# Optimization experiments

Hardware: AMD Instinct MI355X
Metric: run time of the kernel (lower is better)

The kernel has to match this reference:

```python
import jax, jax.numpy as jnp
import numpy as np

NQ, NK, D, DV = 8192, 2048, 2048, 2048

def setup_inputs() -> dict:
    key = jax.random.key(0)
    kq, kk, kv, km = jax.random.split(key, 4)
    Query = jax.random.normal(kq, (NQ, D), dtype=jnp.float32)
    Key = jax.random.normal(kk, (NK, D), dtype=jnp.float32)
    Value = jax.random.normal(kv, (NK, DV), dtype=jnp.float32)
    # binary multiplicative mask (keep prob 0.5); row-all-zero has negligible probability at NK=2048
    mask = (jax.random.uniform(km, (NQ, NK)) > 0.5).astype(jnp.float32)
    return {"Query": Query, "Key": Key, "Value": Value, "mask": mask}

def reference(Query, Key, Value, mask):
    d = Key.shape[1]
    scale = 1.0 / jnp.sqrt(jnp.asarray(d, dtype=Query.dtype))
    scores = jnp.einsum('qd,kd->qk', Query, Key) * scale  # [Nq, Nk]
    energy = jax.nn.softmax(scores, axis=-1) * mask
    att = energy / jnp.sum(energy, axis=-1, keepdims=True)  # renormalize after mask
    return jnp.einsum('qk,kv->qv', att, Value)
```

## Files before the change

### kernel.cpp

```cpp
#include <hip/hip_runtime.h>
#include <hip/hip_bf16.h>


#define NQ 8192
#define NK 2048
#define DD 2048
#define DVV 2048

typedef __attribute__((ext_vector_type(8))) short short8;
typedef __attribute__((ext_vector_type(4))) float f32x4;

typedef __attribute__((address_space(3))) void as3_void;
typedef __attribute__((address_space(1))) const void as1_cvoid;
#define GLOAD16(g, l) __builtin_amdgcn_global_load_lds((as1_cvoid*)(g), (as3_void*)(l), 16, 0, 0)

__global__ __launch_bounds__(256) void conv_bf16_kernel(
    __hip_bfloat16* __restrict__ dst, const float* __restrict__ src, int n4)
{
    int stride = gridDim.x * blockDim.x;
    for (int i = blockIdx.x * blockDim.x + threadIdx.x; i < n4; i += stride) {
        float4 f = reinterpret_cast<const float4*>(src)[i];
        union { __hip_bfloat16 h[4]; uint2 u; } p;
        p.h[0] = __float2bfloat16(f.x);
        p.h[1] = __float2bfloat16(f.y);
        p.h[2] = __float2bfloat16(f.z);
        p.h[3] = __float2bfloat16(f.w);
        reinterpret_cast<uint2*>(dst)[i] = p.u;
    }
}

__global__ __launch_bounds__(256) void transpose_conv_kernel(
    __hip_bfloat16* __restrict__ Vt, const float* __restrict__ V)
{
    __shared__ __hip_bfloat16 tile[64][65];
    const int tx = threadIdx.x;
    const int ty = threadIdx.y;
    const int r0 = blockIdx.y * 64;
    const int c0 = blockIdx.x * 64;
    #pragma unroll
    for (int j = ty; j < 64; j += 4)
        tile[j][tx] = __float2bfloat16(V[(size_t)(r0 + j) * DVV + c0 + tx]);
    __syncthreads();
    #pragma unroll
    for (int j = ty; j < 64; j += 4)
        Vt[(size_t)(c0 + j) * NK + r0 + tx] = tile[tx][j];
}

__global__ __launch_bounds__(256) void gemm_nt_kernel(
    float* __restrict__ C,
    const __hip_bfloat16* __restrict__ A,
    const __hip_bfloat16* __restrict__ B,
    int K, int lda, int ldb, int ldc, float scale)
{
    constexpr int BM = 128, BN = 128, BK = 64;
    __shared__ __align__(16) __hip_bfloat16 As[BM * BK];
    __shared__ __align__(16) __hip_bfloat16 Bs[BN * BK];

    const int tid  = threadIdx.x;
    const int wave = tid >> 6;
    const int lane = tid & 63;
    const int wm   = wave >> 1;
    const int wn   = wave & 1;
    const int bn   = blockIdx.x;
    const int bm   = blockIdx.y;

    f32x4 acc[4][4];
    #pragma unroll
    for (int i = 0; i < 4; ++i)
        #pragma unroll
        for (int j = 0; j < 4; ++j)
            acc[i][j] = (f32x4){0.f, 0.f, 0.f, 0.f};

    const int arow = tid >> 3;
    const int acol = (tid & 7) * 8;
    const __hip_bfloat16* Abase = A + (size_t)(bm * BM + arow) * lda + acol;
    const __hip_bfloat16* Bbase = B + (size_t)(bn * BN + arow) * ldb + acol;

    const int fr = lane & 15;
    const int kb = (lane >> 4) << 3;

    for (int kt = 0; kt < K; kt += BK) {
        __syncthreads();
        #pragma unroll
        for (int r = 0; r < 4; ++r) {
            GLOAD16(Abase + (size_t)(r * 32) * lda + kt, &As[(r * 256 + (wave << 6)) * 8]);
            GLOAD16(Bbase + (size_t)(r * 32) * ldb + kt, &Bs[(r * 256 + (wave << 6)) * 8]);
        }
        __syncthreads();

        #pragma unroll
        for (int kk = 0; kk < 2; ++kk) {
            short8 af[4], bfv[4];
            #pragma unroll
            for (int mi = 0; mi < 4; ++mi)
                af[mi] = *(const short8*)&As[(wm * 64 + mi * 16 + fr) * BK + kk * 32 + kb];
            #pragma unroll
            for (int ni = 0; ni < 4; ++ni)
                bfv[ni] = *(const short8*)&Bs[(wn * 64 + ni * 16 + fr) * BK + kk * 32 + kb];
            #pragma unroll
            for (int mi = 0; mi < 4; ++mi)
                #pragma unroll
                for (int ni = 0; ni < 4; ++ni)
                    acc[mi][ni] = __builtin_amdgcn_mfma_f32_16x16x32_bf16(
                        af[mi], bfv[ni], acc[mi][ni], 0, 0, 0);
        }
    }

    const int crow = bm * BM + wm * 64 + ((lane >> 4) << 2);
    const int ccol = bn * BN + wn * 64 + fr;
    #pragma unroll
    for (int mi = 0; mi < 4; ++mi)
        #pragma unroll
        for (int ni = 0; ni < 4; ++ni)
            #pragma unroll
            for (int r = 0; r < 4; ++r)
                C[(size_t)(crow + mi * 16 + r) * ldc + ccol + ni * 16] = acc[mi][ni][r] * scale;
}

__global__ __launch_bounds__(256) void softmax_mask_kernel(
    float* __restrict__ S, const float* __restrict__ mask)
{
    const int q    = blockIdx.x;
    const int t    = threadIdx.x;
    const int wave = t >> 6;
    const int lane = t & 63;

    const float4* srow = (const float4*)(S + (size_t)q * NK);
    const float4* mrow = (const float4*)(mask + (size_t)q * NK);
    float4 s0 = srow[t], s1 = srow[t + 256];
    float4 m0 = mrow[t], m1 = mrow[t + 256];

    float mx = fmaxf(fmaxf(fmaxf(s0.x, s0.y), fmaxf(s0.z, s0.w)),
                     fmaxf(fmaxf(s1.x, s1.y), fmaxf(s1.z, s1.w)));
    #pragma unroll
    for (int off = 32; off > 0; off >>= 1)
        mx = fmaxf(mx, __shfl_xor(mx, off));

    __shared__ float redm[4], reds[4];
    if (lane == 0) redm[wave] = mx;
    __syncthreads();
    mx = fmaxf(fmaxf(redm[0], redm[1]), fmaxf(redm[2], redm[3]));

    float e[8];
    e[0] = __expf(s0.x - mx) * m0.x;
    e[1] = __expf(s0.y - mx) * m0.y;
    e[2] = __expf(s0.z - mx) * m0.z;
    e[3] = __expf(s0.w - mx) * m0.w;
    e[4] = __expf(s1.x - mx) * m1.x;
    e[5] = __expf(s1.y - mx) * m1.y;
    e[6] = __expf(s1.z - mx) * m1.z;
    e[7] = __expf(s1.w - mx) * m1.w;

    float sum = ((e[0] + e[1]) + (e[2] + e[3])) + ((e[4] + e[5]) + (e[6] + e[7]));
    #pragma unroll
    for (int off = 32; off > 0; off >>= 1)
        sum += __shfl_xor(sum, off);
    if (lane == 0) reds[wave] = sum;
    __syncthreads();
    sum = (reds[0] + reds[1]) + (reds[2] + reds[3]);
    const float inv = 1.0f / sum;

    __hip_bfloat16* prow = reinterpret_cast<__hip_bfloat16*>(S) + (size_t)q * (2 * NK);
    union { __hip_bfloat16 h[4]; uint2 u; } p;
    p.h[0] = __float2bfloat16(e[0] * inv);
    p.h[1] = __float2bfloat16(e[1] * inv);
    p.h[2] = __float2bfloat16(e[2] * inv);
    p.h[3] = __float2bfloat16(e[3] * inv);
    reinterpret_cast<uint2*>(prow)[t] = p.u;
    p.h[0] = __float2bfloat16(e[4] * inv);
    p.h[1] = __float2bfloat16(e[5] * inv);
    p.h[2] = __float2bfloat16(e[6] * inv);
    p.h[3] = __float2bfloat16(e[7] * inv);
    reinterpret_cast<uint2*>(prow)[t + 256] = p.u;
}

extern "C" void kernel_launch(void* const* d_in, const int* in_sizes, int n_in,
                              void* d_out, int out_size, void* d_ws, size_t ws_size,
                              hipStream_t stream)
{
    const float* Q    = (const float*)d_in[0];
    const float* Km   = (const float*)d_in[1];
    const float* V    = (const float*)d_in[2];
    const float* mask = (const float*)d_in[3];
    float* out = (float*)d_out;

    char* ws = (char*)d_ws;
    __hip_bfloat16* Qb  = (__hip_bfloat16*)ws;
    __hip_bfloat16* Kb  = (__hip_bfloat16*)(ws + (size_t)32 * 1024 * 1024);
    __hip_bfloat16* Vtb = (__hip_bfloat16*)(ws + (size_t)40 * 1024 * 1024);
    float*          S   = (float*)        (ws + (size_t)48 * 1024 * 1024);

    conv_bf16_kernel<<<2048, 256, 0, stream>>>(Qb, Q, NQ * DD / 4);
    conv_bf16_kernel<<<1024, 256, 0, stream>>>(Kb, Km, NK * DD / 4);
    transpose_conv_kernel<<<dim3(DVV / 64, NK / 64), dim3(64, 4), 0, stream>>>(Vtb, V);

    const float scale = 0.022097086912079608f;
    gemm_nt_kernel<<<dim3(NK / 128, NQ / 128), 256, 0, stream>>>(
        S, Qb, Kb, DD, DD, DD, NK, scale);
    softmax_mask_kernel<<<NQ, 256, 0, stream>>>(S, mask);
    gemm_nt_kernel<<<dim3(DVV / 128, NQ / 128), 256, 0, stream>>>(
        out, (const __hip_bfloat16*)S, Vtb, NK, 2 * NK, NK, DVV, 1.0f);
}
```

Before: 394.4 us.

## Rewrite GEMM as 256x256 double-buffered 8-wave kernel with swizzled LDS

Replaces the 128x128 single-buffered GEMM with a 256x256 tile, 512-thread kernel that double-buffers LDS and interleaves global-to-LDS loads with MFMA quadrants, using XOR-swizzled LDS layout to avoid bank conflicts and a block-index swizzle for L2 locality. Aims to hide memory latency and raise arithmetic intensity per tile. Larger LDS footprint and register use reduce occupancy and add complexity in wait counts and barrier placement; the grid shrinks to 256 blocks, exactly one wave of work on the device.

After: 330.8 us. -16.1%, faster.

```diff
diff --git a/kernel.cpp b/kernel.cpp
--- a/kernel.cpp
+++ b/kernel.cpp
@@ -13,6 +13,9 @@
 typedef __attribute__((address_space(3))) void as3_void;
 typedef __attribute__((address_space(1))) const void as1_cvoid;
 #define GLOAD16(g, l) __builtin_amdgcn_global_load_lds((as1_cvoid*)(g), (as3_void*)(l), 16, 0, 0)
+
+#define SBAR do { __builtin_amdgcn_sched_barrier(0); __builtin_amdgcn_s_barrier(); } while (0)
+#define WLG0 do { asm volatile("s_waitcnt lgkmcnt(0)" ::: "memory"); __builtin_amdgcn_sched_barrier(0); } while (0)
 
 __global__ __launch_bounds__(256) void conv_bf16_kernel(
     __hip_bfloat16* __restrict__ dst, const float* __restrict__ src, int n4)
@@ -46,75 +49,143 @@
         Vt[(size_t)(c0 + j) * NK + r0 + tx] = tile[tx][j];
 }
 
-__global__ __launch_bounds__(256) void gemm_nt_kernel(
+__global__ __launch_bounds__(512, 2) void gemm_nt8_kernel(
     float* __restrict__ C,
     const __hip_bfloat16* __restrict__ A,
     const __hip_bfloat16* __restrict__ B,
     int K, int lda, int ldb, int ldc, float scale)
 {
-    constexpr int BM = 128, BN = 128, BK = 64;
-    __shared__ __align__(16) __hip_bfloat16 As[BM * BK];
-    __shared__ __align__(16) __hip_bfloat16 Bs[BN * BK];
+    constexpr int BM = 256, BN = 256, BK = 64;
+    const int NT = K / BK;
+    __shared__ __align__(16) __hip_bfloat16 As[2][BM * BK];
+    __shared__ __align__(16) __hip_bfloat16 Bs[2][BN * BK];
 
     const int tid  = threadIdx.x;
     const int wave = tid >> 6;
     const int lane = tid & 63;
-    const int wm   = wave >> 1;
-    const int wn   = wave & 1;
-    const int bn   = blockIdx.x;
-    const int bm   = blockIdx.y;
-
-    f32x4 acc[4][4];
-    #pragma unroll
-    for (int i = 0; i < 4; ++i)
+    const int wm   = wave >> 2;
+    const int wn   = wave & 3;
+    const int fr   = lane & 15;
+    const int fq   = lane >> 4;
+
+    const int swz = (blockIdx.x & 7) * 32 + (blockIdx.x >> 3);
+    const int bm  = swz >> 3;
+    const int bn  = swz & 7;
+
+    const int srow = tid >> 3;
+    const int scol = (((tid & 7) ^ (srow & 7)) << 3);
+
+    const __hip_bfloat16* Ab = A + (size_t)(bm * BM) * lda;
+    const __hip_bfloat16* Bb = B + (size_t)(bn * BN) * ldb;
+
+    f32x4 acc[8][4];
+    #pragma unroll
+    for (int i = 0; i < 8; ++i)
         #pragma unroll
         for (int j = 0; j < 4; ++j)
             acc[i][j] = (f32x4){0.f, 0.f, 0.f, 0.f};
 
-    const int arow = tid >> 3;
-    const int acol = (tid & 7) * 8;
-    const __hip_bfloat16* Abase = A + (size_t)(bm * BM + arow) * lda + acol;
-    const __hip_bfloat16* Bbase = B + (size_t)(bn * BN + arow) * ldb + acol;
-
-    const int fr = lane & 15;
-    const int kb = (lane >> 4) << 3;
-
-    for (int kt = 0; kt < K; kt += BK) {
-        __syncthreads();
-        #pragma unroll
-        for (int r = 0; r < 4; ++r) {
-            GLOAD16(Abase + (size_t)(r * 32) * lda + kt, &As[(r * 256 + (wave << 6)) * 8]);
-            GLOAD16(Bbase + (size_t)(r * 32) * ldb + kt, &Bs[(r * 256 + (wave << 6)) * 8]);
-        }
-        __syncthreads();
-
-        #pragma unroll
-        for (int kk = 0; kk < 2; ++kk) {
-            short8 af[4], bfv[4];
+    short8 af[4][2], b0[2][2], b1[2][2];
+
+    auto stage_a = [&](int pp, int h, int kt) {
+        GLOAD16(Ab + (size_t)(h * 128 +      srow) * lda + kt + scol,
+                &As[pp][(h * 1024 +       wave * 64) * 8]);
+        GLOAD16(Ab + (size_t)(h * 128 + 64 + srow) * lda + kt + scol,
+                &As[pp][(h * 1024 + 512 + wave * 64) * 8]);
+    };
+    auto stage_b = [&](int pp, int h, int kt) {
+        GLOAD16(Bb + (size_t)(h * 128 +      srow) * ldb + kt + scol,
+                &Bs[pp][(h * 1024 +       wave * 64) * 8]);
+        GLOAD16(Bb + (size_t)(h * 128 + 64 + srow) * ldb + kt + scol,
+                &Bs[pp][(h * 1024 + 512 + wave * 64) * 8]);
+    };
+    auto load_a = [&](int pp, int mh) {
+        #pragma unroll
+        for (int mi = 0; mi < 4; ++mi)
             #pragma unroll
-            for (int mi = 0; mi < 4; ++mi)
-                af[mi] = *(const short8*)&As[(wm * 64 + mi * 16 + fr) * BK + kk * 32 + kb];
+            for (int kk = 0; kk < 2; ++kk) {
+                const int row = mh * 128 + wm * 64 + mi * 16 + fr;
+                af[mi][kk] = *(const short8*)
+                    &As[pp][row * 64 + ((((kk << 2) | fq) ^ (fr & 7)) << 3)];
+            }
+    };
+    auto load_b = [&](int pp, int nh, short8 (&dst)[2][2]) {
+        #pragma unroll
+        for (int ni = 0; ni < 2; ++ni)
             #pragma unroll
-            for (int ni = 0; ni < 4; ++ni)
-                bfv[ni] = *(const short8*)&Bs[(wn * 64 + ni * 16 + fr) * BK + kk * 32 + kb];
-            #pragma unroll
-            for (int mi = 0; mi < 4; ++mi)
-                #pragma unroll
-                for (int ni = 0; ni < 4; ++ni)
-                    acc[mi][ni] = __builtin_amdgcn_mfma_f32_16x16x32_bf16(
-                        af[mi], bfv[ni], acc[mi][ni], 0, 0, 0);
-        }
-    }
-
-    const int crow = bm * BM + wm * 64 + ((lane >> 4) << 2);
-    const int ccol = bn * BN + wn * 64 + fr;
-    #pragma unroll
-    for (int mi = 0; mi < 4; ++mi)
-        #pragma unroll
-        for (int ni = 0; ni < 4; ++ni)
+            for (int kk = 0; kk < 2; ++kk) {
+                const int row = nh * 128 + wn * 32 + ni * 16 + fr;
+                dst[ni][kk] = *(const short8*)
+                    &Bs[pp][row * 64 + ((((kk << 2) | fq) ^ (fr & 7)) << 3)];
+            }
+    };
+
+#define QUAD(mh, nh, bset) do {                                              \
+        __builtin_amdgcn_s_setprio(1);                                       \
+        _Pragma("unroll")                                                    \
+        for (int mi = 0; mi < 4; ++mi)                                       \
+            _Pragma("unroll")                                                \
+            for (int ni = 0; ni < 2; ++ni)                                   \
+                _Pragma("unroll")                                            \
+                for (int kk = 0; kk < 2; ++kk)                               \
+                    acc[(mh) * 4 + mi][(nh) * 2 + ni] =                      \
+                        __builtin_amdgcn_mfma_f32_16x16x32_bf16(             \
+                            af[mi][kk], bset[ni][kk],                        \
+                            acc[(mh) * 4 + mi][(nh) * 2 + ni], 0, 0, 0);     \
+        __builtin_amdgcn_s_setprio(0);                                       \
+    } while (0)
+
+    stage_a(0, 0, 0); stage_b(0, 0, 0);
+    stage_a(0, 1, 0); stage_b(0, 1, 0);
+    if (NT > 1) {
+        stage_a(1, 0, BK); stage_b(1, 0, BK);
+        asm volatile("s_waitcnt vmcnt(4)" ::: "memory");
+    } else {
+        asm volatile("s_waitcnt vmcnt(0)" ::: "memory");
+    }
+    SBAR;
+
+    for (int t = 0; t < NT; ++t) {
+        const int p  = t & 1;
+        const int q  = p ^ 1;
+        const int k1 = (t + 1) * BK;
+        const int k2 = (t + 2) * BK;
+        load_a(p, 0);
+        load_b(p, 0, b0);
+        if (t + 1 < NT) stage_a(q, 1, k1);
+        SBAR; WLG0;
+        QUAD(0, 0, b0);
+        SBAR;
+        load_b(p, 1, b1);
+        if (t + 1 < NT) stage_b(q, 1, k1);
+        SBAR; WLG0;
+        QUAD(0, 1, b1);
+        SBAR;
+        load_a(p, 1);
+        if (t + 2 < NT) stage_a(p, 0, k2);
+        SBAR; WLG0;
+        QUAD(1, 0, b0);
+        SBAR;
+        if (t + 2 < NT) stage_b(p, 0, k2);
+        SBAR;
+        QUAD(1, 1, b1);
+        if (t + 2 < NT) { asm volatile("s_waitcnt vmcnt(4)" ::: "memory"); }
+        else            { asm volatile("s_waitcnt vmcnt(0)" ::: "memory"); }
+        SBAR;
+    }
+#undef QUAD
+
+    #pragma unroll
+    for (int mi = 0; mi < 8; ++mi) {
+        const int row = bm * BM + (mi >> 2) * 128 + wm * 64 + (mi & 3) * 16 + fq * 4;
+        #pragma unroll
+        for (int ni = 0; ni < 4; ++ni) {
+            const int col = bn * BN + (ni >> 1) * 128 + wn * 32 + (ni & 1) * 16 + fr;
             #pragma unroll
             for (int r = 0; r < 4; ++r)
-                C[(size_t)(crow + mi * 16 + r) * ldc + ccol + ni * 16] = acc[mi][ni][r] * scale;
+                C[(size_t)(row + r) * ldc + col] = acc[mi][ni][r] * scale;
+        }
+    }
 }
 
 __global__ __launch_bounds__(256) void softmax_mask_kernel(
@@ -195,9 +266,8 @@
     transpose_conv_kernel<<<dim3(DVV / 64, NK / 64), dim3(64, 4), 0, stream>>>(Vtb, V);
 
     const float scale = 0.022097086912079608f;
-    gemm_nt_kernel<<<dim3(NK / 128, NQ / 128), 256, 0, stream>>>(
-        S, Qb, Kb, DD, DD, DD, NK, scale);
+    gemm_nt8_kernel<<<256, 512, 0, stream>>>(S, Qb, Kb, DD, DD, DD, NK, scale);
     softmax_mask_kernel<<<NQ, 256, 0, stream>>>(S, mask);
-    gemm_nt_kernel<<<dim3(DVV / 128, NQ / 128), 256, 0, stream>>>(
-        out, (const __hip_bfloat16*)S, Vtb, NK, 2 * NK, NK, DVV, 1.0f);
-}
+    gemm_nt8_kernel<<<256, 512, 0, stream>>>(out, (const __hip_bfloat16*)S, Vtb,
+                                             NK, 2 * NK, NK, DVV, 1.0f);
+}
```
